# Kernel tuning notes

Measured on AMD Instinct MI355X. Metric: run time of the kernel, lower is better.

## Reference

```python
import jax, jax.numpy as jnp
import numpy as np

BN_EPS = 1e-5


def _conv(x, w, stride, pad):
    return jax.lax.conv_general_dilated(
        x, w, (stride, stride), [(pad, pad), (pad, pad)],
        dimension_numbers=('NCHW', 'OIHW', 'NCHW'))


def setup_inputs() -> dict:
    key = jax.random.key(0)
    ks = jax.random.split(key, 6)
    b, c, h, w = 8, 32, 80, 160
    guidance = jax.random.normal(ks[0], (b, c, 2 * h, 2 * w), dtype=jnp.float32)
    # positive disparities, realistic magnitude
    disp = jax.random.uniform(ks[1], (b, 1, h, w), dtype=jnp.float32) * 24.0
    conv1_w = jax.random.normal(ks[2], (2 * c, c, 3, 3), dtype=jnp.float32) * 0.05
    bn_gamma = jnp.ones((2 * c,), dtype=jnp.float32)
    bn_beta = jnp.zeros((2 * c,), dtype=jnp.float32)
    bn_mean = jax.random.normal(ks[3], (2 * c,), dtype=jnp.float32) * 0.1
    bn_var = jax.random.uniform(ks[4], (2 * c,), dtype=jnp.float32, minval=0.5, maxval=1.5)
    conv2_w = jax.random.normal(ks[5], (9 * 64, 2 * c, 3, 3), dtype=jnp.float32) * 0.05
    return {'guidance': guidance, 'disp': disp, 'conv1_w': conv1_w,
            'bn_gamma': bn_gamma, 'bn_beta': bn_beta, 'bn_mean': bn_mean,
            'bn_var': bn_var, 'conv2_w': conv2_w}


def reference(guidance, disp, conv1_w, bn_gamma, bn_beta, bn_mean, bn_var, conv2_w):
    b, _, h, w = disp.shape
    # mask branch: convbn(stride 2) + ReLU + conv -> 9*64 channels at (h, w)
    x = _conv(guidance, conv1_w, 2, 1)
    inv = jax.lax.rsqrt(bn_var + BN_EPS)
    x = (x - bn_mean[None, :, None, None]) * (inv * bn_gamma)[None, :, None, None] + bn_beta[None, :, None, None]
    x = jax.nn.relu(x)
    mask = _conv(x, conv2_w, 1, 1).reshape(b, 1, 9, 8, 8, h, w)
    mask = jax.nn.softmax(mask, axis=2)
    # unfold(8*disp, 3x3, pad=1) -> (b, 1, 9, h, w), row-major kernel order
    d8 = jnp.pad(8.0 * disp, ((0, 0), (0, 0), (1, 1), (1, 1)))
    patches = jnp.stack([d8[:, :, i:i + h, j:j + w]
                         for i in range(3) for j in range(3)], axis=2)
    # convex combination over the 9 neighbors
    up = jnp.sum(mask * patches[:, :, :, None, None], axis=2)  # (b,1,8,8,h,w)
    up = up.transpose(0, 1, 4, 2, 5, 3)  # (b,1,h,8,w,8)
    return up.reshape(b, 1, 8 * h, 8 * w)
```

## Files before the change

### kernel.cpp

```cpp
#include <hip/hip_runtime.h>
#include <math.h>

typedef _Float16 half8 __attribute__((ext_vector_type(8)));
typedef float f32x4 __attribute__((ext_vector_type(4)));

constexpr int B_ = 8;
constexpr int HG = 160, WG = 320;
constexpr int H = 80, W = 160;
constexpr size_t CWS_OFF  = 0;
constexpr size_t W1WS_OFF = 663552;
constexpr size_t XG_OFF   = 700416;

__device__ __host__ inline int swz_pos(int n, int kl) {
    return ((n >> 1) * 128) + 16 * ((((n & 1) << 2) + (kl >> 3)) ^ ((n >> 1) & 7)) + ((kl & 7) << 1);
}

__global__ __launch_bounds__(256) void prep(const float* __restrict__ w1,
                                            const float* __restrict__ w2,
                                            char* __restrict__ ws)
{
    int e = blockIdx.x * 256 + threadIdx.x;
    if (e < 18 * 576 * 32) {
        int s = e / (576 * 32), rem = e % (576 * 32);
        int n = rem >> 5, kl = rem & 31;
        int cin = (s & 1) * 32 + kl, t = s >> 1;
        int k = n >> 6, ij = n & 63;
        int ng = ij >> 4, nl16 = ij & 15;
        float v = w2[(n * 64 + cin) * 9 + t];
        size_t off = (size_t)ng * 165888 + (size_t)(s * 9 + k) * 1024
                   + ((kl >> 3) * 16 + nl16) * 16 + (kl & 7) * 2;
        *(_Float16*)(ws + CWS_OFF + off) = (_Float16)v;
    } else {
        int e2 = e - 18 * 576 * 32;
        if (e2 < 9 * 64 * 32) {
            int s = e2 / 2048, rem = e2 % 2048;
            int ch = rem >> 5, kl = rem & 31;
            float v = w1[(ch * 32 + kl) * 9 + s];
            *(_Float16*)(ws + W1WS_OFF + (size_t)s * 4096 + swz_pos(ch, kl)) = (_Float16)v;
        }
    }
}

__global__ __launch_bounds__(256) void conv1_mfma(
    const float* __restrict__ g, const char* __restrict__ ws_w1,
    const float* __restrict__ gamma, const float* __restrict__ beta,
    const float* __restrict__ mean, const float* __restrict__ var,
    _Float16* __restrict__ xg)
{
    const int tx0 = blockIdx.x * 8, ty0 = blockIdx.y * 8, b = blockIdx.z;
    __shared__ __align__(16) _Float16 gl[17 * 17 * 40];
    __shared__ __align__(16) _Float16 wlds[64 * 32];
    const int tid = threadIdx.x;
    const _Float16* w1ws = (const _Float16*)ws_w1;

    for (int idx = tid; idx < 17 * 32 * 17; idx += 256) {
        int rr = idx / (32 * 17); int rem = idx - rr * (32 * 17);
        int cin = rem / 17, cc = rem - cin * 17;
        int gy = 2 * ty0 - 1 + rr, gx = 2 * tx0 - 1 + cc;
        float v = 0.f;
        if (gy >= 0 && gy < HG && gx >= 0 && gx < WG)
            v = g[((size_t)(b * 32 + cin) * HG + gy) * WG + gx];
        gl[(rr * 17 + cc) * 40 + cin] = (_Float16)v;
    }

    const int lane = tid & 63, wid = tid >> 6;
    const int wm = wid & 1, wn = wid >> 1;
    const int c = lane & 15, grp = lane >> 4;
    const int slot = ((((c & 1) << 2) + grp) ^ ((c >> 1) & 7));
    const int bbase = wn * 1024 + (c >> 1) * 64 + slot * 8;

    f32x4 zf = {0.f, 0.f, 0.f, 0.f};
    f32x4 acc[2][2];
    acc[0][0] = zf; acc[0][1] = zf; acc[1][0] = zf; acc[1][1] = zf;

    half8 stg = *(const half8*)(w1ws + tid * 8);

#pragma unroll
    for (int s = 0; s < 9; ++s) {
        __syncthreads();
        *(half8*)&wlds[tid * 8] = stg;
        __syncthreads();
        if (s < 8) stg = *(const half8*)(w1ws + (s + 1) * 2048 + tid * 8);
        const int dy = s / 3, dx = s - dy * 3;
        half8 af[2];
#pragma unroll
        for (int mt = 0; mt < 2; ++mt) {
            int rr = 2 * (wm * 4 + mt * 2 + (c >> 3)) + dy;
            int cc2 = 2 * (c & 7) + dx;
            af[mt] = *(const half8*)&gl[(rr * 17 + cc2) * 40 + grp * 8];
        }
#pragma unroll
        for (int nt = 0; nt < 2; ++nt) {
            half8 bf = *(const half8*)&wlds[nt * 512 + bbase];
            acc[0][nt] = __builtin_amdgcn_mfma_f32_16x16x32_f16(af[0], bf, acc[0][nt], 0, 0, 0);
            acc[1][nt] = __builtin_amdgcn_mfma_f32_16x16x32_f16(af[1], bf, acc[1][nt], 0, 0, 0);
        }
    }

#pragma unroll
    for (int nt = 0; nt < 2; ++nt) {
        int ch = wn * 32 + nt * 16 + c;
        float mu = mean[ch], scv = rsqrtf(var[ch] + 1e-5f) * gamma[ch], bt = beta[ch];
#pragma unroll
        for (int mt = 0; mt < 2; ++mt) {
#pragma unroll
            for (int r = 0; r < 4; ++r) {
                int p = wm * 32 + mt * 16 + grp * 4 + r;
                int y = ty0 + (p >> 3), xc = tx0 + (p & 7);
                float v = (acc[mt][nt][r] - mu) * scv + bt;
                v = fmaxf(v, 0.f);
                xg[(((size_t)(b * H + y) * W + xc) << 6) + ch] = (_Float16)v;
            }
        }
    }
}

__global__ __launch_bounds__(256, 2) void conv2_mfma(
    const _Float16* __restrict__ xg, const char* __restrict__ ws_c,
    const float* __restrict__ disp, float* __restrict__ out)
{
    const int tx0 = blockIdx.x * 16, ty0 = blockIdx.y * 4, b = blockIdx.z;
    __shared__ __align__(16) _Float16 xs[108 * 64];
    __shared__ float d8s[108];
    const int tid = threadIdx.x;
    const int lane = tid & 63, wid = tid >> 6;

    half8 zero8;
#pragma unroll
    for (int j = 0; j < 8; ++j) zero8[j] = (_Float16)0.f;
    for (int cidx = tid; cidx < 864; cidx += 256) {
        int wp = cidx >> 3, slot = cidx & 7;
        int rr = wp / 18, cc = wp - rr * 18;
        int y = ty0 - 1 + rr, xc = tx0 - 1 + cc;
        half8 v = zero8;
        if (y >= 0 && y < H && xc >= 0 && xc < W)
            v = *(const half8*)(xg + (((size_t)(b * H + y) * W + xc) << 6) + slot * 8);
        *(half8*)&xs[wp * 64 + (slot ^ (wp & 7)) * 8] = v;
    }
    if (tid < 108) {
        int rr = tid / 18, cc = tid - rr * 18;
        int y = ty0 - 1 + rr, xc = tx0 - 1 + cc;
        float v = 0.f;
        if (y >= 0 && y < H && xc >= 0 && xc < W) v = 8.f * disp[(b * H + y) * W + xc];
        d8s[tid] = v;
    }

    const int c = lane & 15, grp = lane >> 4;

    f32x4 zf = {0.f, 0.f, 0.f, 0.f};
    f32x4 acc[4][9];
#pragma unroll
    for (int m = 0; m < 4; ++m)
#pragma unroll
        for (int k = 0; k < 9; ++k) acc[m][k] = zf;

    const _Float16* wp = (const _Float16*)ws_c + (size_t)wid * 82944 + lane * 8;

    half8 bf[9];
#pragma unroll
    for (int k = 0; k < 9; ++k) bf[k] = *(const half8*)(wp + k * 512);

    __syncthreads();

#pragma unroll 2
    for (int s = 0; s < 18; ++s) {
        const int t = s >> 1;
        const int dy = t / 3, dx = t - dy * 3;
        const int aslot = (s & 1) * 4 + grp;
        half8 af[4];
#pragma unroll
        for (int mt = 0; mt < 4; ++mt) {
            int wrow = (mt + dy) * 18 + c + dx;
            af[mt] = *(const half8*)&xs[wrow * 64 + (aslot ^ (wrow & 7)) * 8];
        }
        const _Float16* wnext = wp + (size_t)(s + 1) * 4608;
#pragma unroll
        for (int k = 0; k < 9; ++k) {
            half8 cur = bf[k];
            bf[k] = *(const half8*)(wnext + k * 512);
#pragma unroll
            for (int mt = 0; mt < 4; ++mt)
                acc[mt][k] = __builtin_amdgcn_mfma_f32_16x16x32_f16(
                    af[mt], cur, acc[mt][k], 0, 0, 0);
        }
    }

    const int ij = wid * 16 + c;
    const int oi = ij >> 3, oj = ij & 7;
#pragma unroll
    for (int mt = 0; mt < 4; ++mt) {
#pragma unroll
        for (int r = 0; r < 4; ++r) {
            int pr = mt, pc = grp * 4 + r;
            float pat[9];
#pragma unroll
            for (int k9 = 0; k9 < 9; ++k9) pat[k9] = d8s[(pr + k9 / 3) * 18 + pc + k9 % 3];
            float mx = acc[mt][0][r];
#pragma unroll
            for (int k9 = 1; k9 < 9; ++k9) mx = fmaxf(mx, acc[mt][k9][r]);
            float sum = 0.f, up = 0.f;
#pragma unroll
            for (int k9 = 0; k9 < 9; ++k9) {
                float e = __expf(acc[mt][k9][r] - mx);
                sum += e; up += e * pat[k9];
            }
            int y = ty0 + pr, xc = tx0 + pc;
            out[((size_t)(b * (8 * H) + y * 8 + oi)) * (size_t)(8 * W) + xc * 8 + oj] = up / sum;
        }
    }
}

extern "C" void kernel_launch(void* const* d_in, const int* in_sizes, int n_in,
                              void* d_out, int out_size, void* d_ws, size_t ws_size,
                              hipStream_t stream)
{
    const float* guidance = (const float*)d_in[0];
    const float* disp     = (const float*)d_in[1];
    const float* conv1_w  = (const float*)d_in[2];
    const float* bn_gamma = (const float*)d_in[3];
    const float* bn_beta  = (const float*)d_in[4];
    const float* bn_mean  = (const float*)d_in[5];
    const float* bn_var   = (const float*)d_in[6];
    const float* conv2_w  = (const float*)d_in[7];
    float* out = (float*)d_out;
    char* ws = (char*)d_ws;
    _Float16* xg = (_Float16*)(ws + XG_OFF);

    prep<<<dim3((18 * 576 * 32 + 9 * 64 * 32 + 255) / 256), dim3(256), 0, stream>>>(
        conv1_w, conv2_w, ws);
    dim3 grid1(W / 8, H / 8, B_);
    conv1_mfma<<<grid1, dim3(256), 0, stream>>>(
        guidance, ws + W1WS_OFF, bn_gamma, bn_beta, bn_mean, bn_var, xg);
    dim3 grid2(W / 16, H / 4, B_);
    conv2_mfma<<<grid2, dim3(256), 0, stream>>>(
        xg, ws + CWS_OFF, disp, out);
}
```

Baseline: 125.0 us.

## Restructure conv1 tiling with float2 loads, widen conv2 to 512 threads, coalesce prep

The conv1 kernel now covers 16x8 output tiles. It loads guidance with float2 reads split by column parity into swizzled LDS, and keeps all four N-tiles of weights in registers prefetched from global memory, which drops the per-tap LDS weight staging and barriers. The conv2 kernel doubles its block to 512 threads covering 8 rows, so the B-fragment weight stream is shared across two M-groups and the halo overhead shrinks. The prep kernel is reorganised so each thread reads contiguous 9-tap weight rows. In exchange, the larger blocks and register arrays raise register pressure and may lower occupancy.

```diff
diff --git a/kernel.cpp b/kernel.cpp
--- a/kernel.cpp
+++ b/kernel.cpp
@@ -11,124 +11,134 @@
 constexpr size_t W1WS_OFF = 663552;
 constexpr size_t XG_OFF   = 700416;
 
-__device__ __host__ inline int swz_pos(int n, int kl) {
-    return ((n >> 1) * 128) + 16 * ((((n & 1) << 2) + (kl >> 3)) ^ ((n >> 1) & 7)) + ((kl & 7) << 1);
-}
-
 __global__ __launch_bounds__(256) void prep(const float* __restrict__ w1,
                                             const float* __restrict__ w2,
                                             char* __restrict__ ws)
 {
     int e = blockIdx.x * 256 + threadIdx.x;
-    if (e < 18 * 576 * 32) {
-        int s = e / (576 * 32), rem = e % (576 * 32);
-        int n = rem >> 5, kl = rem & 31;
-        int cin = (s & 1) * 32 + kl, t = s >> 1;
-        int k = n >> 6, ij = n & 63;
-        int ng = ij >> 4, nl16 = ij & 15;
-        float v = w2[(n * 64 + cin) * 9 + t];
-        size_t off = (size_t)ng * 165888 + (size_t)(s * 9 + k) * 1024
-                   + ((kl >> 3) * 16 + nl16) * 16 + (kl & 7) * 2;
-        *(_Float16*)(ws + CWS_OFF + off) = (_Float16)v;
-    } else {
-        int e2 = e - 18 * 576 * 32;
-        if (e2 < 9 * 64 * 32) {
-            int s = e2 / 2048, rem = e2 % 2048;
-            int ch = rem >> 5, kl = rem & 31;
-            float v = w1[(ch * 32 + kl) * 9 + s];
-            *(_Float16*)(ws + W1WS_OFF + (size_t)s * 4096 + swz_pos(ch, kl)) = (_Float16)v;
-        }
-    }
-}
-
-__global__ __launch_bounds__(256) void conv1_mfma(
+    if (e < 576 * 64) {
+        int n = e >> 6, cin = e & 63;
+        int k = n >> 6, ng = (n >> 4) & 3, nl = n & 15;
+        int kl = cin & 31, c5 = cin >> 5;
+        const float* src = w2 + ((size_t)(n * 64 + cin)) * 9;
+        int fragoff = ((kl >> 3) * 16 + nl) * 16 + (kl & 7) * 2;
+#pragma unroll
+        for (int t = 0; t < 9; ++t) {
+            int s = t * 2 + c5;
+            *(_Float16*)(ws + CWS_OFF + (size_t)ng * 165888
+                         + (size_t)(s * 9 + k) * 1024 + fragoff) = (_Float16)src[t];
+        }
+    } else if (e < 576 * 64 + 64 * 32) {
+        int e2 = e - 576 * 64;
+        int ch = e2 >> 5, cin = e2 & 31;
+        const float* src = w1 + ((size_t)(ch * 32 + cin)) * 9;
+        int fragoff = (ch >> 4) * 1024 + ((cin >> 3) * 16 + (ch & 15)) * 16 + (cin & 7) * 2;
+#pragma unroll
+        for (int t = 0; t < 9; ++t)
+            *(_Float16*)(ws + W1WS_OFF + (size_t)t * 4096 + fragoff) = (_Float16)src[t];
+    }
+}
+
+__global__ __launch_bounds__(256, 4) void conv1_mfma(
     const float* __restrict__ g, const char* __restrict__ ws_w1,
     const float* __restrict__ gamma, const float* __restrict__ beta,
     const float* __restrict__ mean, const float* __restrict__ var,
     _Float16* __restrict__ xg)
 {
-    const int tx0 = blockIdx.x * 8, ty0 = blockIdx.y * 8, b = blockIdx.z;
-    __shared__ __align__(16) _Float16 gl[17 * 17 * 40];
-    __shared__ __align__(16) _Float16 wlds[64 * 32];
+    const int tx0 = blockIdx.x * 16, ty0 = blockIdx.y * 8, b = blockIdx.z;
+    __shared__ __align__(16) _Float16 gl[2][17][18][32];
     const int tid = threadIdx.x;
-    const _Float16* w1ws = (const _Float16*)ws_w1;
-
-    for (int idx = tid; idx < 17 * 32 * 17; idx += 256) {
-        int rr = idx / (32 * 17); int rem = idx - rr * (32 * 17);
-        int cin = rem / 17, cc = rem - cin * 17;
-        int gy = 2 * ty0 - 1 + rr, gx = 2 * tx0 - 1 + cc;
-        float v = 0.f;
-        if (gy >= 0 && gy < HG && gx >= 0 && gx < WG)
-            v = g[((size_t)(b * 32 + cin) * HG + gy) * WG + gx];
-        gl[(rr * 17 + cc) * 40 + cin] = (_Float16)v;
-    }
-
-    const int lane = tid & 63, wid = tid >> 6;
-    const int wm = wid & 1, wn = wid >> 1;
+
+    const int gy0 = 2 * ty0 - 1;
+    const int gxa0 = 2 * tx0 - 2;
+    for (int i = tid; i < 17 * 32 * 17; i += 256) {
+        int wr = i / 544; int rem = i - wr * 544;
+        int cin = rem / 17; int c2 = rem - cin * 17;
+        int gy = gy0 + wr;
+        int gxa = gxa0 + 2 * c2;
+        float2 v = make_float2(0.f, 0.f);
+        if (gy >= 0 && gy < HG && gxa >= 0)
+            v = *(const float2*)(g + ((size_t)(b * 32 + cin) * HG + gy) * WG + gxa);
+        int slot = cin >> 3, elem = cin & 7;
+        if (c2 > 0) {
+            int wch = c2 - 1;
+            gl[1][wr][wch][((slot ^ ((wch >> 1) & 3)) << 3) + elem] = (_Float16)v.x;
+        }
+        {
+            int wch = c2;
+            gl[0][wr][wch][((slot ^ ((wch >> 1) & 3)) << 3) + elem] = (_Float16)v.y;
+        }
+    }
+
+    const int lane = tid & 63, w = tid >> 6;
     const int c = lane & 15, grp = lane >> 4;
-    const int slot = ((((c & 1) << 2) + grp) ^ ((c >> 1) & 7));
-    const int bbase = wn * 1024 + (c >> 1) * 64 + slot * 8;
+
+    const _Float16* w1p = (const _Float16*)ws_w1 + lane * 8;
+    half8 bf[4];
+#pragma unroll
+    for (int nt = 0; nt < 4; ++nt) bf[nt] = *(const half8*)(w1p + nt * 512);
 
     f32x4 zf = {0.f, 0.f, 0.f, 0.f};
-    f32x4 acc[2][2];
-    acc[0][0] = zf; acc[0][1] = zf; acc[1][0] = zf; acc[1][1] = zf;
-
-    half8 stg = *(const half8*)(w1ws + tid * 8);
+    f32x4 acc[2][4];
+#pragma unroll
+    for (int mt = 0; mt < 2; ++mt)
+#pragma unroll
+        for (int nt = 0; nt < 4; ++nt) acc[mt][nt] = zf;
+
+    __syncthreads();
 
 #pragma unroll
     for (int s = 0; s < 9; ++s) {
-        __syncthreads();
-        *(half8*)&wlds[tid * 8] = stg;
-        __syncthreads();
-        if (s < 8) stg = *(const half8*)(w1ws + (s + 1) * 2048 + tid * 8);
         const int dy = s / 3, dx = s - dy * 3;
+        const int par = dx & 1, dxh = dx >> 1;
         half8 af[2];
 #pragma unroll
         for (int mt = 0; mt < 2; ++mt) {
-            int rr = 2 * (wm * 4 + mt * 2 + (c >> 3)) + dy;
-            int cc2 = 2 * (c & 7) + dx;
-            af[mt] = *(const half8*)&gl[(rr * 17 + cc2) * 40 + grp * 8];
-        }
-#pragma unroll
-        for (int nt = 0; nt < 2; ++nt) {
-            half8 bf = *(const half8*)&wlds[nt * 512 + bbase];
-            acc[0][nt] = __builtin_amdgcn_mfma_f32_16x16x32_f16(af[0], bf, acc[0][nt], 0, 0, 0);
-            acc[1][nt] = __builtin_amdgcn_mfma_f32_16x16x32_f16(af[1], bf, acc[1][nt], 0, 0, 0);
-        }
-    }
-
-#pragma unroll
-    for (int nt = 0; nt < 2; ++nt) {
-        int ch = wn * 32 + nt * 16 + c;
+            int wr = 2 * (2 * w + mt) + dy;
+            int wch = c + dxh;
+            af[mt] = *(const half8*)&gl[par][wr][wch][(grp ^ ((wch >> 1) & 3)) << 3];
+        }
+        const _Float16* wnext = w1p + (size_t)(s + 1) * 2048;
+#pragma unroll
+        for (int nt = 0; nt < 4; ++nt) {
+            half8 cur = bf[nt];
+            bf[nt] = *(const half8*)(wnext + nt * 512);
+            acc[0][nt] = __builtin_amdgcn_mfma_f32_16x16x32_f16(af[0], cur, acc[0][nt], 0, 0, 0);
+            acc[1][nt] = __builtin_amdgcn_mfma_f32_16x16x32_f16(af[1], cur, acc[1][nt], 0, 0, 0);
+        }
+    }
+
+#pragma unroll
+    for (int nt = 0; nt < 4; ++nt) {
+        int ch = nt * 16 + c;
         float mu = mean[ch], scv = rsqrtf(var[ch] + 1e-5f) * gamma[ch], bt = beta[ch];
 #pragma unroll
         for (int mt = 0; mt < 2; ++mt) {
+            int y = ty0 + 2 * w + mt;
 #pragma unroll
             for (int r = 0; r < 4; ++r) {
-                int p = wm * 32 + mt * 16 + grp * 4 + r;
-                int y = ty0 + (p >> 3), xc = tx0 + (p & 7);
-                float v = (acc[mt][nt][r] - mu) * scv + bt;
-                v = fmaxf(v, 0.f);
-                xg[(((size_t)(b * H + y) * W + xc) << 6) + ch] = (_Float16)v;
+                int x = tx0 + grp * 4 + r;
+                float v = fmaxf((acc[mt][nt][r] - mu) * scv + bt, 0.f);
+                xg[(((size_t)(b * H + y) * W + x) << 6) + ch] = (_Float16)v;
             }
         }
     }
 }
 
-__global__ __launch_bounds__(256, 2) void conv2_mfma(
+__global__ __launch_bounds__(512, 2) void conv2_mfma(
     const _Float16* __restrict__ xg, const char* __restrict__ ws_c,
     const float* __restrict__ disp, float* __restrict__ out)
 {
-    const int tx0 = blockIdx.x * 16, ty0 = blockIdx.y * 4, b = blockIdx.z;
-    __shared__ __align__(16) _Float16 xs[108 * 64];
-    __shared__ float d8s[108];
+    const int tx0 = blockIdx.x * 16, ty0 = blockIdx.y * 8, b = blockIdx.z;
+    __shared__ __align__(16) _Float16 xs[180 * 64];
+    __shared__ float d8s[180];
     const int tid = threadIdx.x;
     const int lane = tid & 63, wid = tid >> 6;
 
     half8 zero8;
 #pragma unroll
     for (int j = 0; j < 8; ++j) zero8[j] = (_Float16)0.f;
-    for (int cidx = tid; cidx < 864; cidx += 256) {
+    for (int cidx = tid; cidx < 1440; cidx += 512) {
         int wp = cidx >> 3, slot = cidx & 7;
         int rr = wp / 18, cc = wp - rr * 18;
         int y = ty0 - 1 + rr, xc = tx0 - 1 + cc;
@@ -137,7 +147,7 @@
             v = *(const half8*)(xg + (((size_t)(b * H + y) * W + xc) << 6) + slot * 8);
         *(half8*)&xs[wp * 64 + (slot ^ (wp & 7)) * 8] = v;
     }
-    if (tid < 108) {
+    if (tid < 180) {
         int rr = tid / 18, cc = tid - rr * 18;
         int y = ty0 - 1 + rr, xc = tx0 - 1 + cc;
         float v = 0.f;
@@ -145,6 +155,7 @@
         d8s[tid] = v;
     }
 
+    const int ng = wid & 3, mg = wid >> 2;
     const int c = lane & 15, grp = lane >> 4;
 
     f32x4 zf = {0.f, 0.f, 0.f, 0.f};
@@ -154,7 +165,7 @@
 #pragma unroll
         for (int k = 0; k < 9; ++k) acc[m][k] = zf;
 
-    const _Float16* wp = (const _Float16*)ws_c + (size_t)wid * 82944 + lane * 8;
+    const _Float16* wp = (const _Float16*)ws_c + (size_t)ng * 82944 + lane * 8;
 
     half8 bf[9];
 #pragma unroll
@@ -170,7 +181,7 @@
         half8 af[4];
 #pragma unroll
         for (int mt = 0; mt < 4; ++mt) {
-            int wrow = (mt + dy) * 18 + c + dx;
+            int wrow = (mg * 4 + mt + dy) * 18 + c + dx;
             af[mt] = *(const half8*)&xs[wrow * 64 + (aslot ^ (wrow & 7)) * 8];
         }
         const _Float16* wnext = wp + (size_t)(s + 1) * 4608;
@@ -185,13 +196,13 @@
         }
     }
 
-    const int ij = wid * 16 + c;
+    const int ij = ng * 16 + c;
     const int oi = ij >> 3, oj = ij & 7;
 #pragma unroll
     for (int mt = 0; mt < 4; ++mt) {
 #pragma unroll
         for (int r = 0; r < 4; ++r) {
-            int pr = mt, pc = grp * 4 + r;
+            int pr = mg * 4 + mt, pc = grp * 4 + r;
             float pat[9];
 #pragma unroll
             for (int k9 = 0; k9 < 9; ++k9) pat[k9] = d8s[(pr + k9 / 3) * 18 + pc + k9 % 3];
@@ -226,12 +237,12 @@
     char* ws = (char*)d_ws;
     _Float16* xg = (_Float16*)(ws + XG_OFF);
 
-    prep<<<dim3((18 * 576 * 32 + 9 * 64 * 32 + 255) / 256), dim3(256), 0, stream>>>(
+    prep<<<dim3((576 * 64 + 64 * 32 + 255) / 256), dim3(256), 0, stream>>>(
         conv1_w, conv2_w, ws);
-    dim3 grid1(W / 8, H / 8, B_);
+    dim3 grid1(W / 16, H / 8, B_);
     conv1_mfma<<<grid1, dim3(256), 0, stream>>>(
         guidance, ws + W1WS_OFF, bn_gamma, bn_beta, bn_mean, bn_var, xg);
-    dim3 grid2(W / 16, H / 4, B_);
-    conv2_mfma<<<grid2, dim3(256), 0, stream>>>(
+    dim3 grid2(W / 16, H / 8, B_);
+    conv2_mfma<<<grid2, dim3(512), 0, stream>>>(
         xg, ws + CWS_OFF, disp, out);
 }
```

Measured after the change: 120.1 us. 1.04x faster.
